# Optimization experiments

Measured on AMD Instinct MI355X. Metric: run time of the kernel, lower is better.

The kernel has to match this reference:

```python
import jax, jax.numpy as jnp
import numpy as np

DIM_MODEL = 1024
DIM_K = 1024
DIM_V = 1024


def setup_inputs() -> dict:
    key = jax.random.key(0)
    ks = jax.random.split(key, 7)
    B, S = 4, 2048
    scale = 1.0 / np.sqrt(DIM_MODEL)
    return {
        "x": jax.random.normal(ks[0], (B, S, DIM_MODEL), dtype=jnp.float32),
        # weights stored [in, out] (transpose of torch Linear.weight)
        "Wq": jax.random.normal(ks[1], (DIM_MODEL, DIM_K), dtype=jnp.float32) * scale,
        "Wk": jax.random.normal(ks[2], (DIM_MODEL, DIM_K), dtype=jnp.float32) * scale,
        "Wv": jax.random.normal(ks[3], (DIM_MODEL, DIM_V), dtype=jnp.float32) * scale,
        "Wo": jax.random.normal(ks[4], (DIM_V, DIM_MODEL), dtype=jnp.float32) * (1.0 / np.sqrt(DIM_V)),
        "ln2_gamma": jnp.ones((DIM_MODEL,), dtype=jnp.float32),
        "ln2_beta": jnp.zeros((DIM_MODEL,), dtype=jnp.float32),
    }


def _layernorm(x, gamma, beta, eps=1e-5):
    mu = jnp.mean(x, axis=-1, keepdims=True)
    var = jnp.var(x, axis=-1, keepdims=True)
    return (x - mu) * jax.lax.rsqrt(var + eps) * gamma + beta


def reference(x, Wq, Wk, Wv, Wo, ln2_gamma, ln2_beta):
    # single-head attention, x: [B,S,D]
    q = jnp.einsum("bsd,dk->bsk", x, Wq)
    k = jnp.einsum("bsd,dk->bsk", x, Wk)
    v = jnp.einsum("bsd,dv->bsv", x, Wv)
    scores = jnp.einsum("bqk,bsk->bqs", q, k) / jnp.sqrt(jnp.asarray(DIM_K, x.dtype))
    attn = jax.nn.softmax(scores, axis=-1)  # [B,S,S]
    ctx = jnp.einsum("bqs,bsv->bqv", attn, v)
    hidden = jnp.einsum("bqv,vd->bqd", ctx, Wo)
    hidden = _layernorm(hidden, ln2_gamma, ln2_beta)
    return hidden
```

## Files before the change

### kernel.cpp

```cpp
#include <hip/hip_runtime.h>
#include <hip/hip_bf16.h>
#include <stdint.h>

typedef __bf16 bf16;
typedef __attribute__((ext_vector_type(8))) __bf16 bf16x8;
typedef __attribute__((ext_vector_type(4))) float f32x4;

#define AS1 __attribute__((address_space(1)))
#define AS3 __attribute__((address_space(3)))

__device__ __forceinline__ void gl_lds16(const void* g, void* l) {
  __builtin_amdgcn_global_load_lds((const AS1 uint32_t*)g, (AS3 uint32_t*)l, 16, 0, 0);
}

template <typename OUT>
__global__ __launch_bounds__(256) void gemm_bt(
    const bf16* __restrict__ Abase, const bf16* __restrict__ Bbase,
    OUT* __restrict__ Cbase, int K, int lda, int ldb, int ldc,
    long long sA, long long sB, long long sC, float alpha) {
  __shared__ bf16 As[128 * 64];
  __shared__ bf16 Bs[128 * 64];
  const int z = blockIdx.z;
  const bf16* A = Abase + (long long)z * sA;
  const bf16* B = Bbase + (long long)z * sB;
  OUT* C = Cbase + (long long)z * sC;
  const int m0 = blockIdx.y * 128, n0 = blockIdx.x * 128;
  const int t = threadIdx.x;
  const int lane = t & 63, wave = t >> 6;
  const int wm = (wave >> 1) * 64, wn = (wave & 1) * 64;
  const int quad = lane >> 4, r = lane & 15;

  const int srow = t >> 3;
  const int schunk = (t & 7) ^ (srow & 7);
  const bf16* ga = A + (long long)(m0 + srow) * lda + schunk * 8;
  const bf16* gb = B + (long long)(n0 + srow) * ldb + schunk * 8;
  char* la = (char*)As + t * 16;
  char* lb = (char*)Bs + t * 16;

  f32x4 acc[4][4] = {};

  for (int k0 = 0; k0 < K; k0 += 64) {
    __syncthreads();
#pragma unroll
    for (int rd = 0; rd < 4; rd++) {
      gl_lds16(ga + (long long)(32 * rd) * lda, la + rd * 4096);
      gl_lds16(gb + (long long)(32 * rd) * ldb, lb + rd * 4096);
    }
    ga += 64;
    gb += 64;
    __syncthreads();

#pragma unroll
    for (int kk = 0; kk < 2; kk++) {
      bf16x8 af[4], bfr[4];
      const int csa = ((kk * 4 + quad) ^ (r & 7)) * 16;
      const char* pa = (const char*)As + (wm + r) * 128 + csa;
      const char* pb = (const char*)Bs + (wn + r) * 128 + csa;
#pragma unroll
      for (int i = 0; i < 4; i++) af[i] = *(const bf16x8*)(pa + i * 2048);
#pragma unroll
      for (int j = 0; j < 4; j++) bfr[j] = *(const bf16x8*)(pb + j * 2048);
#pragma unroll
      for (int i = 0; i < 4; i++)
#pragma unroll
        for (int j = 0; j < 4; j++)
          acc[i][j] = __builtin_amdgcn_mfma_f32_16x16x32_bf16(af[i], bfr[j],
                                                              acc[i][j], 0, 0, 0);
    }
  }

#pragma unroll
  for (int i = 0; i < 4; i++) {
    const int row0 = m0 + wm + i * 16 + quad * 4;
#pragma unroll
    for (int j = 0; j < 4; j++) {
      const int col = n0 + wn + j * 16 + r;
#pragma unroll
      for (int rg = 0; rg < 4; rg++) {
        float v = acc[i][j][rg] * alpha;
        C[(long long)(row0 + rg) * ldc + col] = (OUT)v;
      }
    }
  }
}

__global__ __launch_bounds__(256) void cvt_f32_bf16(
    const float* __restrict__ in, bf16* __restrict__ out, long long n8) {
  long long i = (long long)blockIdx.x * 256 + threadIdx.x;
  if (i >= n8) return;
  const float4* p = (const float4*)in;
  float4 a = p[i * 2], b = p[i * 2 + 1];
  bf16x8 o;
  o[0] = (bf16)a.x; o[1] = (bf16)a.y; o[2] = (bf16)a.z; o[3] = (bf16)a.w;
  o[4] = (bf16)b.x; o[5] = (bf16)b.y; o[6] = (bf16)b.z; o[7] = (bf16)b.w;
  ((bf16x8*)out)[i] = o;
}

__global__ __launch_bounds__(256) void transpose_w4(
    const float* __restrict__ Wq, const float* __restrict__ Wk,
    const float* __restrict__ Wv, const float* __restrict__ Wo,
    bf16* __restrict__ Wcat, bf16* __restrict__ Wot) {
  __shared__ float tile[32][33];
  const int z = blockIdx.z;
  const float* W = (z == 0) ? Wq : (z == 1) ? Wk : (z == 2) ? Wv : Wo;
  bf16* dst = (z < 3) ? (Wcat + (long long)z * 1024 * 1024) : Wot;
  int bx = blockIdx.x * 32, by = blockIdx.y * 32;
  int tx = threadIdx.x & 31, ty = threadIdx.x >> 5;
#pragma unroll
  for (int i = 0; i < 32; i += 8)
    tile[ty + i][tx] = W[(long long)(by + ty + i) * 1024 + bx + tx];
  __syncthreads();
#pragma unroll
  for (int i = 0; i < 32; i += 8)
    dst[(long long)(bx + ty + i) * 1024 + by + tx] = (bf16)tile[tx][ty + i];
}

__global__ __launch_bounds__(256) void transpose_v(
    const bf16* __restrict__ V, bf16* __restrict__ Vt, int ldsrc,
    long long sV) {
  __shared__ bf16 tile[32][33];
  const bf16* Vb = V + (long long)blockIdx.z * sV;
  bf16* Vtb = Vt + (long long)blockIdx.z * 1024 * 2048;
  int bx = blockIdx.x * 32, by = blockIdx.y * 32;
  int tx = threadIdx.x & 31, ty = threadIdx.x >> 5;
#pragma unroll
  for (int i = 0; i < 32; i += 8)
    tile[ty + i][tx] = Vb[(long long)(by + ty + i) * ldsrc + bx + tx];
  __syncthreads();
#pragma unroll
  for (int i = 0; i < 32; i += 8)
    Vtb[(long long)(bx + ty + i) * 2048 + by + tx] = tile[tx][ty + i];
}

__global__ __launch_bounds__(256) void softmax_rows(
    const bf16* __restrict__ S, bf16* __restrict__ P, int n) {
  const long long row = blockIdx.x;
  const int t = threadIdx.x;
  const int lane = t & 63, wave = t >> 6;
  bf16x8 in8 = ((const bf16x8*)(S + row * n))[t];
  float v[8];
#pragma unroll
  for (int i = 0; i < 8; i++) v[i] = (float)in8[i];
  float m = v[0];
#pragma unroll
  for (int i = 1; i < 8; i++) m = fmaxf(m, v[i]);
#pragma unroll
  for (int off = 32; off >= 1; off >>= 1) m = fmaxf(m, __shfl_xor(m, off));
  __shared__ float red[8];
  if (lane == 0) red[wave] = m;
  __syncthreads();
  m = fmaxf(fmaxf(red[0], red[1]), fmaxf(red[2], red[3]));
  float sum = 0.f;
#pragma unroll
  for (int i = 0; i < 8; i++) {
    v[i] = __expf(v[i] - m);
    sum += v[i];
  }
#pragma unroll
  for (int off = 32; off >= 1; off >>= 1) sum += __shfl_xor(sum, off);
  if (lane == 0) red[4 + wave] = sum;
  __syncthreads();
  sum = red[4] + red[5] + red[6] + red[7];
  float inv = 1.f / sum;
  bf16x8 o;
#pragma unroll
  for (int i = 0; i < 8; i++) o[i] = (bf16)(v[i] * inv);
  ((bf16x8*)(P + row * n))[t] = o;
}

__global__ __launch_bounds__(256) void layernorm_rows(
    const float* __restrict__ H, const float* __restrict__ gamma,
    const float* __restrict__ beta, float* __restrict__ O) {
  const long long row = blockIdx.x;
  const float* h = H + row * 1024;
  float* o = O + row * 1024;
  const int t = threadIdx.x;
  const int lane = t & 63, wave = t >> 6;
  float4 v = ((const float4*)h)[t];
  float s = v.x + v.y + v.z + v.w;
  float ss = v.x * v.x + v.y * v.y + v.z * v.z + v.w * v.w;
#pragma unroll
  for (int off = 32; off >= 1; off >>= 1) {
    s += __shfl_xor(s, off);
    ss += __shfl_xor(ss, off);
  }
  __shared__ float rs[4], rss[4];
  if (lane == 0) {
    rs[wave] = s;
    rss[wave] = ss;
  }
  __syncthreads();
  s = rs[0] + rs[1] + rs[2] + rs[3];
  ss = rss[0] + rss[1] + rss[2] + rss[3];
  const float mean = s * (1.f / 1024.f);
  const float var = ss * (1.f / 1024.f) - mean * mean;
  const float rstd = rsqrtf(var + 1e-5f);
  float4 g = ((const float4*)gamma)[t];
  float4 bb = ((const float4*)beta)[t];
  float4 r;
  r.x = (v.x - mean) * rstd * g.x + bb.x;
  r.y = (v.y - mean) * rstd * g.y + bb.y;
  r.z = (v.z - mean) * rstd * g.z + bb.z;
  r.w = (v.w - mean) * rstd * g.w + bb.w;
  ((float4*)o)[t] = r;
}

extern "C" void kernel_launch(void* const* d_in, const int* in_sizes, int n_in,
                              void* d_out, int out_size, void* d_ws,
                              size_t ws_size, hipStream_t stream) {
  const float* x = (const float*)d_in[0];
  const float* Wq = (const float*)d_in[1];
  const float* Wk = (const float*)d_in[2];
  const float* Wv = (const float*)d_in[3];
  const float* Wo = (const float*)d_in[4];
  const float* gamma = (const float*)d_in[5];
  const float* beta = (const float*)d_in[6];
  float* out = (float*)d_out;

  char* ws = (char*)d_ws;
  const size_t MB = 1024ull * 1024ull;
  bf16* Xb = (bf16*)(ws + 0);
  bf16* Wcat = (bf16*)(ws + 16 * MB);
  bf16* Wot = (bf16*)(ws + 22 * MB);
  bf16* QKV = (bf16*)(ws + 24 * MB);
  bf16* Vt = (bf16*)(ws + 72 * MB);
  bf16* S = (bf16*)(ws + 88 * MB);
  bf16* P = (bf16*)(ws + 120 * MB);
  bf16* ctx = (bf16*)(ws + 152 * MB);
  float* Hd = (float*)(ws + 88 * MB);

  const long long bQKV = 2048LL * 3072;

  cvt_f32_bf16<<<4096, 256, 0, stream>>>(x, Xb, 8192LL * 1024 / 8);
  transpose_w4<<<dim3(32, 32, 4), 256, 0, stream>>>(Wq, Wk, Wv, Wo, Wcat, Wot);

  gemm_bt<bf16><<<dim3(24, 64, 1), 256, 0, stream>>>(
      Xb, Wcat, QKV, 1024, 1024, 1024, 3072, 0, 0, 0, 1.f);

  transpose_v<<<dim3(32, 64, 4), 256, 0, stream>>>(QKV + 2048, Vt, 3072, bQKV);

  gemm_bt<bf16><<<dim3(16, 16, 4), 256, 0, stream>>>(
      QKV, QKV + 1024, S, 1024, 3072, 3072, 2048, bQKV, bQKV, 2048 * 2048LL,
      0.03125f);

  softmax_rows<<<8192, 256, 0, stream>>>(S, P, 2048);

  gemm_bt<bf16><<<dim3(8, 16, 4), 256, 0, stream>>>(
      P, Vt, ctx, 2048, 2048, 2048, 1024, 2048 * 2048LL, 1024 * 2048LL,
      2048 * 1024LL, 1.f);

  gemm_bt<float><<<dim3(8, 64, 1), 256, 0, stream>>>(
      ctx, Wot, Hd, 1024, 1024, 1024, 1024, 0, 0, 0, 1.f);

  layernorm_rows<<<8192, 256, 0, stream>>>(Hd, gamma, beta, out);
}
```

Measured before the change: 323.3 us.

## Fuse softmax into QK^T and PV GEMM epilogues with deferred normalization

Removes the standalone softmax kernel. The QK^T GEMM epilogue now writes exp(scores) in bf16 and atomically accumulates row sums into a small buffer. The PV GEMM epilogue divides by those sums. The buffer is zeroed inside the input conversion kernel. The output projection now writes bf16 instead of fp32, which halves the traffic into the layernorm. The cost is skipping max subtraction, so exp can overflow if scores grow large, plus atomic contention and reduced precision before the layernorm.

```diff
diff --git a/kernel.cpp b/kernel.cpp
--- a/kernel.cpp
+++ b/kernel.cpp
@@ -4,6 +4,7 @@
 
 typedef __bf16 bf16;
 typedef __attribute__((ext_vector_type(8))) __bf16 bf16x8;
+typedef __attribute__((ext_vector_type(4))) __bf16 bf16x4;
 typedef __attribute__((ext_vector_type(4))) float f32x4;
 
 #define AS1 __attribute__((address_space(1)))
@@ -13,11 +14,12 @@
   __builtin_amdgcn_global_load_lds((const AS1 uint32_t*)g, (AS3 uint32_t*)l, 16, 0, 0);
 }
 
-template <typename OUT>
+template <typename OUT, int MODE>
 __global__ __launch_bounds__(256) void gemm_bt(
     const bf16* __restrict__ Abase, const bf16* __restrict__ Bbase,
     OUT* __restrict__ Cbase, int K, int lda, int ldb, int ldc,
-    long long sA, long long sB, long long sC, float alpha) {
+    long long sA, long long sB, long long sC, float alpha,
+    float* __restrict__ lsum) {
   __shared__ bf16 As[128 * 64];
   __shared__ bf16 Bs[128 * 64];
   const int z = blockIdx.z;
@@ -72,20 +74,47 @@
 #pragma unroll
   for (int i = 0; i < 4; i++) {
     const int row0 = m0 + wm + i * 16 + quad * 4;
+    float rsum[4] = {0.f, 0.f, 0.f, 0.f};
+    float inv[4];
+    if constexpr (MODE == 2) {
+#pragma unroll
+      for (int rg = 0; rg < 4; rg++)
+        inv[rg] = 1.f / lsum[(long long)z * 2048 + row0 + rg];
+    }
 #pragma unroll
     for (int j = 0; j < 4; j++) {
       const int col = n0 + wn + j * 16 + r;
 #pragma unroll
       for (int rg = 0; rg < 4; rg++) {
         float v = acc[i][j][rg] * alpha;
-        C[(long long)(row0 + rg) * ldc + col] = (OUT)v;
+        if constexpr (MODE == 1) {
+          bf16 eb = (bf16)__expf(v);
+          C[(long long)(row0 + rg) * ldc + col] = (OUT)eb;
+          rsum[rg] += (float)eb;
+        } else if constexpr (MODE == 2) {
+          C[(long long)(row0 + rg) * ldc + col] = (OUT)(v * inv[rg]);
+        } else {
+          C[(long long)(row0 + rg) * ldc + col] = (OUT)v;
+        }
       }
     }
+    if constexpr (MODE == 1) {
+#pragma unroll
+      for (int rg = 0; rg < 4; rg++) {
+#pragma unroll
+        for (int off = 8; off >= 1; off >>= 1)
+          rsum[rg] += __shfl_xor(rsum[rg], off);
+        if (r == 0)
+          atomicAdd(&lsum[(long long)z * 2048 + row0 + rg], rsum[rg]);
+      }
+    }
   }
 }
 
 __global__ __launch_bounds__(256) void cvt_f32_bf16(
-    const float* __restrict__ in, bf16* __restrict__ out, long long n8) {
+    const float* __restrict__ in, bf16* __restrict__ out, long long n8,
+    float* __restrict__ lsum) {
+  if (blockIdx.x < 32) lsum[blockIdx.x * 256 + threadIdx.x] = 0.f;
   long long i = (long long)blockIdx.x * 256 + threadIdx.x;
   if (i >= n8) return;
   const float4* p = (const float4*)in;
@@ -132,53 +161,18 @@
     Vtb[(long long)(bx + ty + i) * 2048 + by + tx] = tile[tx][ty + i];
 }
 
-__global__ __launch_bounds__(256) void softmax_rows(
-    const bf16* __restrict__ S, bf16* __restrict__ P, int n) {
-  const long long row = blockIdx.x;
-  const int t = threadIdx.x;
-  const int lane = t & 63, wave = t >> 6;
-  bf16x8 in8 = ((const bf16x8*)(S + row * n))[t];
-  float v[8];
-#pragma unroll
-  for (int i = 0; i < 8; i++) v[i] = (float)in8[i];
-  float m = v[0];
-#pragma unroll
-  for (int i = 1; i < 8; i++) m = fmaxf(m, v[i]);
-#pragma unroll
-  for (int off = 32; off >= 1; off >>= 1) m = fmaxf(m, __shfl_xor(m, off));
-  __shared__ float red[8];
-  if (lane == 0) red[wave] = m;
-  __syncthreads();
-  m = fmaxf(fmaxf(red[0], red[1]), fmaxf(red[2], red[3]));
-  float sum = 0.f;
-#pragma unroll
-  for (int i = 0; i < 8; i++) {
-    v[i] = __expf(v[i] - m);
-    sum += v[i];
-  }
-#pragma unroll
-  for (int off = 32; off >= 1; off >>= 1) sum += __shfl_xor(sum, off);
-  if (lane == 0) red[4 + wave] = sum;
-  __syncthreads();
-  sum = red[4] + red[5] + red[6] + red[7];
-  float inv = 1.f / sum;
-  bf16x8 o;
-#pragma unroll
-  for (int i = 0; i < 8; i++) o[i] = (bf16)(v[i] * inv);
-  ((bf16x8*)(P + row * n))[t] = o;
-}
-
 __global__ __launch_bounds__(256) void layernorm_rows(
-    const float* __restrict__ H, const float* __restrict__ gamma,
+    const bf16* __restrict__ H, const float* __restrict__ gamma,
     const float* __restrict__ beta, float* __restrict__ O) {
   const long long row = blockIdx.x;
-  const float* h = H + row * 1024;
+  const bf16* h = H + row * 1024;
   float* o = O + row * 1024;
   const int t = threadIdx.x;
   const int lane = t & 63, wave = t >> 6;
-  float4 v = ((const float4*)h)[t];
-  float s = v.x + v.y + v.z + v.w;
-  float ss = v.x * v.x + v.y * v.y + v.z * v.z + v.w * v.w;
+  bf16x4 hv = ((const bf16x4*)h)[t];
+  float v[4] = {(float)hv[0], (float)hv[1], (float)hv[2], (float)hv[3]};
+  float s = v[0] + v[1] + v[2] + v[3];
+  float ss = v[0] * v[0] + v[1] * v[1] + v[2] * v[2] + v[3] * v[3];
 #pragma unroll
   for (int off = 32; off >= 1; off >>= 1) {
     s += __shfl_xor(s, off);
@@ -197,12 +191,12 @@
   const float rstd = rsqrtf(var + 1e-5f);
   float4 g = ((const float4*)gamma)[t];
   float4 bb = ((const float4*)beta)[t];
-  float4 r;
-  r.x = (v.x - mean) * rstd * g.x + bb.x;
-  r.y = (v.y - mean) * rstd * g.y + bb.y;
-  r.z = (v.z - mean) * rstd * g.z + bb.z;
-  r.w = (v.w - mean) * rstd * g.w + bb.w;
-  ((float4*)o)[t] = r;
+  float4 rr;
+  rr.x = (v[0] - mean) * rstd * g.x + bb.x;
+  rr.y = (v[1] - mean) * rstd * g.y + bb.y;
+  rr.z = (v[2] - mean) * rstd * g.z + bb.z;
+  rr.w = (v[3] - mean) * rstd * g.w + bb.w;
+  ((float4*)o)[t] = rr;
 }
 
 extern "C" void kernel_launch(void* const* d_in, const int* in_sizes, int n_in,
@@ -224,33 +218,31 @@
   bf16* Wot = (bf16*)(ws + 22 * MB);
   bf16* QKV = (bf16*)(ws + 24 * MB);
   bf16* Vt = (bf16*)(ws + 72 * MB);
-  bf16* S = (bf16*)(ws + 88 * MB);
-  bf16* P = (bf16*)(ws + 120 * MB);
-  bf16* ctx = (bf16*)(ws + 152 * MB);
-  float* Hd = (float*)(ws + 88 * MB);
+  bf16* expS = (bf16*)(ws + 88 * MB);
+  float* lsum = (float*)(ws + 120 * MB);
+  bf16* ctx = (bf16*)(ws + 121 * MB);
+  bf16* Hd = (bf16*)(ws + 137 * MB);
 
   const long long bQKV = 2048LL * 3072;
 
-  cvt_f32_bf16<<<4096, 256, 0, stream>>>(x, Xb, 8192LL * 1024 / 8);
+  cvt_f32_bf16<<<4096, 256, 0, stream>>>(x, Xb, 8192LL * 1024 / 8, lsum);
   transpose_w4<<<dim3(32, 32, 4), 256, 0, stream>>>(Wq, Wk, Wv, Wo, Wcat, Wot);
 
-  gemm_bt<bf16><<<dim3(24, 64, 1), 256, 0, stream>>>(
-      Xb, Wcat, QKV, 1024, 1024, 1024, 3072, 0, 0, 0, 1.f);
+  gemm_bt<bf16, 0><<<dim3(24, 64, 1), 256, 0, stream>>>(
+      Xb, Wcat, QKV, 1024, 1024, 1024, 3072, 0, 0, 0, 1.f, nullptr);
 
   transpose_v<<<dim3(32, 64, 4), 256, 0, stream>>>(QKV + 2048, Vt, 3072, bQKV);
 
-  gemm_bt<bf16><<<dim3(16, 16, 4), 256, 0, stream>>>(
-      QKV, QKV + 1024, S, 1024, 3072, 3072, 2048, bQKV, bQKV, 2048 * 2048LL,
-      0.03125f);
-
-  softmax_rows<<<8192, 256, 0, stream>>>(S, P, 2048);
-
-  gemm_bt<bf16><<<dim3(8, 16, 4), 256, 0, stream>>>(
-      P, Vt, ctx, 2048, 2048, 2048, 1024, 2048 * 2048LL, 1024 * 2048LL,
-      2048 * 1024LL, 1.f);
-
-  gemm_bt<float><<<dim3(8, 64, 1), 256, 0, stream>>>(
-      ctx, Wot, Hd, 1024, 1024, 1024, 1024, 0, 0, 0, 1.f);
+  gemm_bt<bf16, 1><<<dim3(16, 16, 4), 256, 0, stream>>>(
+      QKV, QKV + 1024, expS, 1024, 3072, 3072, 2048, bQKV, bQKV,
+      2048 * 2048LL, 0.03125f, lsum);
+
+  gemm_bt<bf16, 2><<<dim3(8, 16, 4), 256, 0, stream>>>(
+      expS, Vt, ctx, 2048, 2048, 2048, 1024, 2048 * 2048LL, 1024 * 2048LL,
+      2048 * 1024LL, 1.f, lsum);
+
+  gemm_bt<bf16, 0><<<dim3(8, 64, 1), 256, 0, stream>>>(
+      ctx, Wot, Hd, 1024, 1024, 1024, 1024, 0, 0, 0, 1.f, nullptr);
 
   layernorm_rows<<<8192, 256, 0, stream>>>(Hd, gamma, beta, out);
 }
```

Measured after the change: 311.9 us. -3.5%, faster.
